# Kernel optimization log

Hardware: AMD Instinct MI355X
Metric: run time of the kernel (lower is better)

Reference implementation:

```python
import jax, jax.numpy as jnp
import numpy as np

N_ROI, N_GRAPHS, HID, EDIM, EMB, NGRP = 116, 128, 64, 5, 16, 4
IN_CH, OUT_CH, N_LAYERS = 116, 2, 2


def _seg_softmax(scores, seg, num_segments):
    # numerically stable softmax over edges grouped by target node
    m = jax.ops.segment_max(scores, seg, num_segments=num_segments)
    ex = jnp.exp(scores - m[seg])
    s = jax.ops.segment_sum(ex, seg, num_segments=num_segments)
    return ex / (s[seg] + 1e-16)


def setup_inputs():
    key = jax.random.key(0)
    ks = jax.random.split(key, 16)
    N = N_ROI * N_GRAPHS
    idx = np.arange(N_ROI)
    s = np.repeat(idx, N_ROI)
    d = np.tile(idx, N_ROI)
    off = (np.arange(N_GRAPHS) * N_ROI)[:, None]
    src = (s[None, :] + off).reshape(-1)
    dst = (d[None, :] + off).reshape(-1)
    E = src.size

    def W(i, shp):
        fan = shp[-2] if len(shp) >= 2 else shp[-1]
        return jax.random.normal(ks[i], shp, jnp.float32) / np.sqrt(fan)

    def z(*shp):
        return jnp.zeros(shp, jnp.float32)

    return {
        "x": jax.random.normal(ks[0], (N, IN_CH), jnp.float32),
        "edge_attr": jax.random.normal(ks[1], (E, EDIM), jnp.float32),
        "emb": W(2, (NGRP, EMB)),
        "enc_W": W(3, (IN_CH + EMB, HID)), "enc_b": z(HID),
        "bn_g": jnp.ones((HID,), jnp.float32), "bn_b": z(HID),
        "gine_We": W(4, (EDIM, HID)), "gine_be": z(HID),
        "gine_W1": W(5, (HID, HID)), "gine_b1": z(HID),
        "gine_W2": W(6, (HID, HID)), "gine_b2": z(HID),
        "gat_Wl": W(7, (N_LAYERS, HID, HID)), "gat_bl": z(N_LAYERS, HID),
        "gat_Wr": W(8, (N_LAYERS, HID, HID)), "gat_br": z(N_LAYERS, HID),
        "gat_att": W(9, (N_LAYERS, HID)),
        "gat_We": W(10, (N_LAYERS, EDIM, HID)),
        "gat_bias": z(N_LAYERS, HID),
        "pool_W1": W(11, (HID, HID)), "pool_b1": z(HID), "pool_w2": W(12, (HID,)),
        "lin1_W": W(13, (HID, IN_CH)), "lin1_b": z(IN_CH),
        "lin2_W": W(14, (IN_CH, OUT_CH)), "lin2_b": z(OUT_CH),
        "edge_index": jnp.asarray(np.stack([src, dst]), jnp.int32),
        "batch": jnp.asarray(np.repeat(np.arange(N_GRAPHS), N_ROI), jnp.int32),
        "group_ids": jnp.asarray(np.tile(idx // 29, N_GRAPHS), jnp.int32),
        "num_graphs": N_GRAPHS,
    }


def reference(x, edge_attr, emb, enc_W, enc_b, bn_g, bn_b,
              gine_We, gine_be, gine_W1, gine_b1, gine_W2, gine_b2,
              gat_Wl, gat_bl, gat_Wr, gat_br, gat_att, gat_We, gat_bias,
              pool_W1, pool_b1, pool_w2, lin1_W, lin1_b, lin2_W, lin2_b,
              edge_index, batch, group_ids, num_graphs):
    src, dst = edge_index[0], edge_index[1]
    N = x.shape[0]
    # BrainEncodeEmbed: concat group embedding, linear, batchnorm (batch stats)
    h = jnp.concatenate([x, emb[group_ids]], axis=-1)          # [N, IN_CH+EMB]
    h = jax.nn.relu(h @ enc_W + enc_b)                          # [N, HID]
    mu = h.mean(0)
    var = h.var(0)
    h = (h - mu) * jax.lax.rsqrt(var + 1e-5) * bn_g + bn_b
    # GINEConv (eps=0): sum_j relu(x_j + lin_edge(e_ij)), then MLP
    e = edge_attr @ gine_We + gine_be                           # [E, HID]
    agg = jax.ops.segment_sum(jax.nn.relu(h[src] + e), dst, num_segments=N)
    h = h + agg
    h = jax.nn.relu(h @ gine_W1 + gine_b1) @ gine_W2 + gine_b2
    h = jax.nn.relu(h)
    # GATv2 layers (heads=1, concat=False)
    for l in range(N_LAYERS):
        xl = h @ gat_Wl[l] + gat_bl[l]                          # [N, HID]
        xr = h @ gat_Wr[l] + gat_br[l]
        zed = jax.nn.leaky_relu(xl[src] + xr[dst] + edge_attr @ gat_We[l], 0.2)
        alpha = _seg_softmax(zed @ gat_att[l], dst, N)          # [E]
        h = jax.nn.relu(
            jax.ops.segment_sum(xl[src] * alpha[:, None], dst, num_segments=N)
            + gat_bias[l])
    # AttentionPooling: global softmax over all nodes, scatter-add by graph
    w = jax.nn.softmax(jnp.tanh(h @ pool_W1 + pool_b1) @ pool_w2, axis=0)
    pooled = jax.ops.segment_sum(h * w[:, None], batch, num_segments=num_graphs)
    return jax.nn.relu(pooled @ lin1_W + lin1_b) @ lin2_W + lin2_b
```

## Files before the change

### kernel.cpp

```cpp
#include <hip/hip_runtime.h>
#include <math.h>

#define R    116
#define R2   (116*116)
#define G    128
#define NN   (R*G)
#define HID  64
#define EDIM 5
#define INCH 116
#define EMBD 16

__device__ __forceinline__ float waveReduceSum(float v) {
#pragma unroll
    for (int m = 32; m >= 1; m >>= 1) v += __shfl_xor(v, m, 64);
    return v;
}

__global__ __launch_bounds__(256) void k_etr(
    const float* __restrict__ ea, float* __restrict__ eat) {
    int b = blockIdx.x;
    int g = b >> 4;
    int t = b & 15;
    int i0 = (t >> 2) << 5, j0 = (t & 3) << 5;
    int ni = min(32, R - i0), nj = min(32, R - j0);
    __shared__ float tile[32][165];
    const float* src = ea + ((size_t)(g*R + i0)*R + j0)*EDIM;
    int tot = ni * nj * EDIM;
    for (int idx = threadIdx.x; idx < tot; idx += 256) {
        int ii = idx / (nj*EDIM);
        int rem = idx - ii*(nj*EDIM);
        tile[ii][rem] = src[(size_t)ii*R*EDIM + rem];
    }
    __syncthreads();
    float* dst = eat + ((size_t)(g*R + j0)*R + i0)*EDIM;
    int tot2 = nj * ni * EDIM;
    for (int idx = threadIdx.x; idx < tot2; idx += 256) {
        int jj = idx / (ni*EDIM);
        int rem = idx - jj*(ni*EDIM);
        int ii = rem / EDIM, e = rem - ii*EDIM;
        dst[(size_t)jj*R*EDIM + rem] = tile[ii][jj*EDIM + e];
    }
}

__global__ __launch_bounds__(64) void k_prep(
    const float* __restrict__ We, const float* __restrict__ att,
    float* __restrict__ wepack, float* __restrict__ was2) {
    int l = blockIdx.x, c = threadIdx.x;
    const float* Wl = We + l*EDIM*HID;
    const float* al = att + l*HID;
    float g0=Wl[c], g1=Wl[64+c], g2=Wl[128+c], g3=Wl[192+c], g4=Wl[256+c];
    float at = al[c];
    float* wp = wepack + l*HID*8 + c*8;
    wp[0]=g0; wp[1]=g1; wp[2]=g2; wp[3]=g3; wp[4]=g4; wp[5]=at;
    wp[6]=0.f; wp[7]=0.f;
    float p0 = waveReduceSum(g0*at);
    float p1 = waveReduceSum(g1*at);
    float p2 = waveReduceSum(g2*at);
    float p3 = waveReduceSum(g3*at);
    float p4 = waveReduceSum(g4*at);
    if (c == 0) {
        float* ws = was2 + l*8;
        ws[0]=p0; ws[1]=p1; ws[2]=p2; ws[3]=p3; ws[4]=p4;
    }
}

__global__ __launch_bounds__(256) void k_encode(
    const float* __restrict__ x, const float* __restrict__ emb,
    const int* __restrict__ group_ids,
    const float* __restrict__ W, const float* __restrict__ bvec,
    float* __restrict__ h) {
    int w = threadIdx.x >> 6, lane = threadIdx.x & 63;
    int n = blockIdx.x*4 + w;
    __shared__ float xin[4][136];
    for (int idx = lane; idx < INCH; idx += 64) xin[w][idx] = x[(size_t)n*INCH + idx];
    if (lane < EMBD) xin[w][INCH + lane] = emb[group_ids[n]*EMBD + lane];
    float acc = bvec[lane];
#pragma unroll
    for (int k = 0; k < INCH + EMBD; k += 4) {
        float4 q = *(const float4*)&xin[w][k];
        acc = fmaf(q.x, W[(k  )*HID + lane], acc);
        acc = fmaf(q.y, W[(k+1)*HID + lane], acc);
        acc = fmaf(q.z, W[(k+2)*HID + lane], acc);
        acc = fmaf(q.w, W[(k+3)*HID + lane], acc);
    }
    h[(size_t)n*HID + lane] = fmaxf(acc, 0.f);
}

__global__ __launch_bounds__(256) void k_stats_partial(
    const float* __restrict__ h, float* __restrict__ partials) {
    int b = blockIdx.x;
    int tid = threadIdx.x;
    int c = tid & 63, r0 = tid >> 6;
    float s = 0.f, s2 = 0.f;
    int row0 = b*64;
#pragma unroll
    for (int k = 0; k < 16; ++k) {
        float v = h[(size_t)(row0 + r0 + 4*k)*HID + c];
        s += v; s2 += v*v;
    }
    __shared__ float ls[256], l2[256];
    ls[tid] = s; l2[tid] = s2;
    __syncthreads();
    if (tid < 64) {
        s  = ls[tid] + ls[tid+64] + ls[tid+128] + ls[tid+192];
        s2 = l2[tid] + l2[tid+64] + l2[tid+128] + l2[tid+192];
        partials[b*128 + tid]      = s;
        partials[b*128 + 64 + tid] = s2;
    }
}

__global__ __launch_bounds__(64) void k_stats_final(
    const float* __restrict__ partials, const float* __restrict__ gam,
    const float* __restrict__ bet, float* __restrict__ stats) {
    int c = threadIdx.x;
    float s = 0.f, s2 = 0.f;
    for (int b = 0; b < NN/64; ++b) {
        s  += partials[b*128 + c];
        s2 += partials[b*128 + 64 + c];
    }
    float mu  = s / (float)NN;
    float var = s2 / (float)NN - mu*mu;
    float rs  = rsqrtf(var + 1e-5f);
    float sc  = rs * gam[c];
    stats[c]      = sc;
    stats[64 + c] = bet[c] - mu*sc;
}

__global__ __launch_bounds__(256) void k_gine(
    const float* __restrict__ h, const float* __restrict__ stats,
    const float* __restrict__ ea,
    const float* __restrict__ We, const float* __restrict__ be,
    const float* __restrict__ W1, const float* __restrict__ b1,
    const float* __restrict__ W2, const float* __restrict__ b2,
    float* __restrict__ hout) {
    int b = blockIdx.x;
    int g = b & (G-1), q = b >> 7;
    int tid = threadIdx.x, w = tid >> 6, lane = tid & 63;
    int j0 = min(q*32 + w*8, R - 8);
    __shared__ float hs[R][64];
    __shared__ float t1s[4][68];
    size_t hbase = (size_t)g*R*HID;
    float scv = stats[lane], shv = stats[64 + lane];
    for (int idx = tid; idx < R*HID; idx += 256)
        hs[idx>>6][lane] = fmaf(h[hbase + idx], scv, shv);
    float w0=We[lane], w1v=We[64+lane], w2v=We[128+lane],
          w3v=We[192+lane], w4v=We[256+lane], bec=be[lane];
    __syncthreads();

    float acc[8] = {0.f,0.f,0.f,0.f,0.f,0.f,0.f,0.f};
    int sbase = __builtin_amdgcn_readfirstlane((g*R*R + j0)*EDIM);
    for (int i = 0; i < R; ++i) {
        float hv = hs[i][lane];
        const float* sp = ea + sbase + i*(R*EDIM);
#pragma unroll
        for (int j = 0; j < 8; ++j) {
            float ew = bec;
            ew = fmaf(sp[j*5+0], w0,  ew);
            ew = fmaf(sp[j*5+1], w1v, ew);
            ew = fmaf(sp[j*5+2], w2v, ew);
            ew = fmaf(sp[j*5+3], w3v, ew);
            ew = fmaf(sp[j*5+4], w4v, ew);
            acc[j] += fmaxf(hv + ew, 0.f);
        }
    }
#pragma unroll
    for (int j = 0; j < 8; ++j) {
        int jd = j0 + j;
        float h1 = hs[jd][lane] + acc[j];
        t1s[w][lane] = h1;
        float a1 = b1[lane];
#pragma unroll
        for (int k = 0; k < HID; k += 4) {
            float4 tq = *(const float4*)&t1s[w][k];
            a1 = fmaf(tq.x, W1[(k  )*HID + lane], a1);
            a1 = fmaf(tq.y, W1[(k+1)*HID + lane], a1);
            a1 = fmaf(tq.z, W1[(k+2)*HID + lane], a1);
            a1 = fmaf(tq.w, W1[(k+3)*HID + lane], a1);
        }
        t1s[w][lane] = fmaxf(a1, 0.f);
        float a2 = b2[lane];
#pragma unroll
        for (int k = 0; k < HID; k += 4) {
            float4 tq = *(const float4*)&t1s[w][k];
            a2 = fmaf(tq.x, W2[(k  )*HID + lane], a2);
            a2 = fmaf(tq.y, W2[(k+1)*HID + lane], a2);
            a2 = fmaf(tq.z, W2[(k+2)*HID + lane], a2);
            a2 = fmaf(tq.w, W2[(k+3)*HID + lane], a2);
        }
        hout[hbase + (size_t)jd*HID + lane] = fmaxf(a2, 0.f);
    }
}

__global__ __launch_bounds__(256) void k_xlxr(
    const float* __restrict__ h,
    const float* __restrict__ Wl, const float* __restrict__ bl,
    const float* __restrict__ Wr, const float* __restrict__ br,
    const float* __restrict__ att,
    float* __restrict__ xl, float* __restrict__ xr,
    float* __restrict__ axl, float* __restrict__ axr) {
    int w = threadIdx.x >> 6, lane = threadIdx.x & 63;
    int n = blockIdx.x*4 + w;
    __shared__ float hr[4][68];
    hr[w][lane] = h[(size_t)n*HID + lane];
    float aL = bl[lane], aR = br[lane];
#pragma unroll
    for (int k = 0; k < HID; k += 4) {
        float4 q = *(const float4*)&hr[w][k];
        aL = fmaf(q.x, Wl[(k  )*HID + lane], aL);
        aR = fmaf(q.x, Wr[(k  )*HID + lane], aR);
        aL = fmaf(q.y, Wl[(k+1)*HID + lane], aL);
        aR = fmaf(q.y, Wr[(k+1)*HID + lane], aR);
        aL = fmaf(q.z, Wl[(k+2)*HID + lane], aL);
        aR = fmaf(q.z, Wr[(k+2)*HID + lane], aR);
        aL = fmaf(q.w, Wl[(k+3)*HID + lane], aL);
        aR = fmaf(q.w, Wr[(k+3)*HID + lane], aR);
    }
    xl[(size_t)n*HID + lane] = aL;
    xr[(size_t)n*HID + lane] = aR;
    float at = att[lane];
    float pL = waveReduceSum(aL * at);
    float pR = waveReduceSum(aR * at);
    if (lane == 0) { axl[n] = pL; axr[n] = pR; }
}

__global__ __launch_bounds__(256) void k_gat(
    const float* __restrict__ xl, const float* __restrict__ xr,
    const float* __restrict__ axlg, const float* __restrict__ axrg,
    const float* __restrict__ eat, const float* __restrict__ wepack,
    const float* __restrict__ wasg, const float* __restrict__ bias,
    float* __restrict__ hout) {
    int b = blockIdx.x;
    int g = b & (G-1), chunk = b >> 7;
    int j0 = chunk*15, jcnt = min(15, R - j0);
    int tid = threadIdx.x, w = tid >> 6, lane = tid & 63;
    __shared__ float xls[R][66];
    __shared__ float ps[4][120];
    size_t hbase = (size_t)g*R*HID;
    for (int idx = tid; idx < R*HID; idx += 256)
        xls[idx>>6][idx&63] = xl[hbase + idx];
    float biasv = bias[lane];
    float wasv0 = wasg[0], wasv1 = wasg[1], wasv2 = wasg[2],
          wasv3 = wasg[3], wasv4 = wasg[4];
    bool vB = lane < (R - 64);
    int rb = vB ? (64 + lane) : lane;
    float axA = axlg[g*R + lane];
    float axB = axlg[g*R + rb];
    __syncthreads();

    for (int jj = w; jj < jcnt; jj += 4) {
        int j = j0 + jj;
        const float* colp = eat + (size_t)(g*R + j)*R*EDIM;
        float eA[5], eB[5];
#pragma unroll
        for (int e = 0; e < 5; ++e) {
            eA[e] = colp[lane*EDIM + e];
            eB[e] = colp[rb*EDIM + e];
        }
        const float* xrp = xr + hbase + (size_t)j*HID;
        float axrj = axrg[g*R + j];
        float accA = 0.f, accB = 0.f;
#pragma unroll 4
        for (int c = 0; c < HID; c += 2) {
            float2 xA2 = *(const float2*)&xls[lane][c];
            float2 xB2 = *(const float2*)&xls[rb][c];
            {
                const float* wp = wepack + c*8;
                float u = xrp[c];
                float zA = xA2.x + u;
                zA = fmaf(eA[0],wp[0],zA); zA = fmaf(eA[1],wp[1],zA);
                zA = fmaf(eA[2],wp[2],zA); zA = fmaf(eA[3],wp[3],zA);
                zA = fmaf(eA[4],wp[4],zA);
                accA = fmaf(__builtin_fabsf(zA), wp[5], accA);
                float zB = xB2.x + u;
                zB = fmaf(eB[0],wp[0],zB); zB = fmaf(eB[1],wp[1],zB);
                zB = fmaf(eB[2],wp[2],zB); zB = fmaf(eB[3],wp[3],zB);
                zB = fmaf(eB[4],wp[4],zB);
                accB = fmaf(__builtin_fabsf(zB), wp[5], accB);
            }
            {
                const float* wp = wepack + (c+1)*8;
                float u = xrp[c+1];
                float zA = xA2.y + u;
                zA = fmaf(eA[0],wp[0],zA); zA = fmaf(eA[1],wp[1],zA);
                zA = fmaf(eA[2],wp[2],zA); zA = fmaf(eA[3],wp[3],zA);
                zA = fmaf(eA[4],wp[4],zA);
                accA = fmaf(__builtin_fabsf(zA), wp[5], accA);
                float zB = xB2.y + u;
                zB = fmaf(eB[0],wp[0],zB); zB = fmaf(eB[1],wp[1],zB);
                zB = fmaf(eB[2],wp[2],zB); zB = fmaf(eB[3],wp[3],zB);
                zB = fmaf(eB[4],wp[4],zB);
                accB = fmaf(__builtin_fabsf(zB), wp[5], accB);
            }
        }
        float LA = axA + axrj, LB = axB + axrj;
        LA = fmaf(eA[0],wasv0,LA); LA = fmaf(eA[1],wasv1,LA);
        LA = fmaf(eA[2],wasv2,LA); LA = fmaf(eA[3],wasv3,LA);
        LA = fmaf(eA[4],wasv4,LA);
        LB = fmaf(eB[0],wasv0,LB); LB = fmaf(eB[1],wasv1,LB);
        LB = fmaf(eB[2],wasv2,LB); LB = fmaf(eB[3],wasv3,LB);
        LB = fmaf(eB[4],wasv4,LB);
        float sA = fmaf(0.4f, accA, 0.6f*LA);
        float sB = vB ? fmaf(0.4f, accB, 0.6f*LB) : -1e30f;
        float m = fmaxf(sA, sB);
#pragma unroll
        for (int msk = 32; msk >= 1; msk >>= 1) m = fmaxf(m, __shfl_xor(m, msk, 64));
        float eAx = __expf(sA - m);
        float eBx = vB ? __expf(sB - m) : 0.f;
        float s = eAx + eBx;
#pragma unroll
        for (int msk = 32; msk >= 1; msk >>= 1) s += __shfl_xor(s, msk, 64);
        float inv = 1.f / (s + 1e-16f);
        ps[w][lane] = eAx * inv;
        if (vB) ps[w][64 + lane] = eBx * inv;
        float o = 0.f;
#pragma unroll 4
        for (int i = 0; i < R; i += 4) {
            float4 p4 = *(const float4*)&ps[w][i];
            o = fmaf(p4.x, xls[i  ][lane], o);
            o = fmaf(p4.y, xls[i+1][lane], o);
            o = fmaf(p4.z, xls[i+2][lane], o);
            o = fmaf(p4.w, xls[i+3][lane], o);
        }
        hout[hbase + (size_t)j*HID + lane] = fmaxf(o + biasv, 0.f);
    }
}

__global__ __launch_bounds__(256) void k_pool_score(
    const float* __restrict__ h, const float* __restrict__ W1,
    const float* __restrict__ b1, const float* __restrict__ w2,
    float* __restrict__ scores) {
    int w = threadIdx.x >> 6, lane = threadIdx.x & 63;
    int n = blockIdx.x*4 + w;
    __shared__ float hr[4][68];
    hr[w][lane] = h[(size_t)n*HID + lane];
    float acc = b1[lane];
#pragma unroll
    for (int k = 0; k < HID; k += 4) {
        float4 q = *(const float4*)&hr[w][k];
        acc = fmaf(q.x, W1[(k  )*HID + lane], acc);
        acc = fmaf(q.y, W1[(k+1)*HID + lane], acc);
        acc = fmaf(q.z, W1[(k+2)*HID + lane], acc);
        acc = fmaf(q.w, W1[(k+3)*HID + lane], acc);
    }
    float p = tanhf(acc) * w2[lane];
    p = waveReduceSum(p);
    if (lane == 0) scores[n] = p;
}

__global__ __launch_bounds__(1024) void k_pool_reduce(
    const float* __restrict__ scores, float* __restrict__ ms) {
    __shared__ float red[1024];
    int tid = threadIdx.x;
    float m = -1e30f;
    for (int i = tid; i < NN; i += 1024) m = fmaxf(m, scores[i]);
    red[tid] = m;
    __syncthreads();
    for (int s = 512; s > 0; s >>= 1) {
        if (tid < s) red[tid] = fmaxf(red[tid], red[tid+s]);
        __syncthreads();
    }
    float mx = red[0];
    __syncthreads();
    float sum = 0.f;
    for (int i = tid; i < NN; i += 1024) sum += __expf(scores[i] - mx);
    red[tid] = sum;
    __syncthreads();
    for (int s = 512; s > 0; s >>= 1) {
        if (tid < s) red[tid] += red[tid+s];
        __syncthreads();
    }
    if (tid == 0) { ms[0] = mx; ms[1] = red[0]; }
}

__global__ __launch_bounds__(64) void k_pool_final(
    const float* __restrict__ h, const float* __restrict__ scores,
    const float* __restrict__ ms,
    const float* __restrict__ lin1W, const float* __restrict__ lin1b,
    const float* __restrict__ lin2W, const float* __restrict__ lin2b,
    float* __restrict__ out) {
    int g = blockIdx.x, c = threadIdx.x;
    float mx = ms[0], inv = 1.f / ms[1];
    float pc = 0.f;
    int nb = g*R;
    for (int r = 0; r < R; ++r) {
        float wv = __expf(scores[nb + r] - mx) * inv;
        pc = fmaf(h[(size_t)(nb + r)*HID + c], wv, pc);
    }
    __shared__ float pl[HID];
    __shared__ float t[INCH];
    pl[c] = pc;
    __syncthreads();
    for (int k = c; k < INCH; k += 64) {
        float acc = lin1b[k];
#pragma unroll 8
        for (int q = 0; q < HID; ++q) acc = fmaf(pl[q], lin1W[q*INCH + k], acc);
        t[k] = fmaxf(acc, 0.f);
    }
    __syncthreads();
    if (c < 2) {
        float o = lin2b[c];
        for (int k = 0; k < INCH; ++k) o = fmaf(t[k], lin2W[k*2 + c], o);
        out[g*2 + c] = o;
    }
}

extern "C" void kernel_launch(void* const* d_in, const int* in_sizes, int n_in,
                              void* d_out, int out_size, void* d_ws, size_t ws_size,
                              hipStream_t stream) {
    (void)in_sizes; (void)n_in; (void)out_size; (void)ws_size;
    const float* x        = (const float*)d_in[0];
    const float* edge_attr= (const float*)d_in[1];
    const float* emb      = (const float*)d_in[2];
    const float* enc_W    = (const float*)d_in[3];
    const float* enc_b    = (const float*)d_in[4];
    const float* bn_g     = (const float*)d_in[5];
    const float* bn_b     = (const float*)d_in[6];
    const float* gine_We  = (const float*)d_in[7];
    const float* gine_be  = (const float*)d_in[8];
    const float* gine_W1  = (const float*)d_in[9];
    const float* gine_b1  = (const float*)d_in[10];
    const float* gine_W2  = (const float*)d_in[11];
    const float* gine_b2  = (const float*)d_in[12];
    const float* gat_Wl   = (const float*)d_in[13];
    const float* gat_bl   = (const float*)d_in[14];
    const float* gat_Wr   = (const float*)d_in[15];
    const float* gat_br   = (const float*)d_in[16];
    const float* gat_att  = (const float*)d_in[17];
    const float* gat_We   = (const float*)d_in[18];
    const float* gat_bias = (const float*)d_in[19];
    const float* pool_W1  = (const float*)d_in[20];
    const float* pool_b1  = (const float*)d_in[21];
    const float* pool_w2  = (const float*)d_in[22];
    const float* lin1_W   = (const float*)d_in[23];
    const float* lin1_b   = (const float*)d_in[24];
    const float* lin2_W   = (const float*)d_in[25];
    const float* lin2_b   = (const float*)d_in[26];
    const int*   group_ids= (const int*)d_in[29];
    float* out = (float*)d_out;

    float* w = (float*)d_ws;
    float* eat      = w;
    float* hA       = eat + (size_t)R2*G*EDIM;
    float* hB       = hA + (size_t)NN*HID;
    float* xlb      = hB + (size_t)NN*HID;
    float* xrb      = xlb + (size_t)NN*HID;
    float* axl      = xrb + (size_t)NN*HID;
    float* axr      = axl + NN;
    float* scores   = axr + NN;
    float* partials = scores + NN;
    float* stats    = partials + (NN/64)*128;
    float* pms      = stats + 128;
    float* wepack   = pms + 2;
    float* was2     = wepack + 2*HID*8;

    k_etr<<<G*16, 256, 0, stream>>>(edge_attr, eat);
    k_prep<<<2, 64, 0, stream>>>(gat_We, gat_att, wepack, was2);
    k_encode<<<NN/4, 256, 0, stream>>>(x, emb, group_ids, enc_W, enc_b, hA);
    k_stats_partial<<<NN/64, 256, 0, stream>>>(hA, partials);
    k_stats_final<<<1, 64, 0, stream>>>(partials, bn_g, bn_b, stats);
    k_gine<<<G*4, 256, 0, stream>>>(hA, stats, edge_attr, gine_We, gine_be,
                                    gine_W1, gine_b1, gine_W2, gine_b2, hB);
    k_xlxr<<<NN/4, 256, 0, stream>>>(hB, gat_Wl, gat_bl, gat_Wr, gat_br,
                                     gat_att, xlb, xrb, axl, axr);
    k_gat<<<G*8, 256, 0, stream>>>(xlb, xrb, axl, axr, eat, wepack,
                                   was2, gat_bias, hA);
    k_xlxr<<<NN/4, 256, 0, stream>>>(hA, gat_Wl + HID*HID, gat_bl + HID,
                                     gat_Wr + HID*HID, gat_br + HID,
                                     gat_att + HID, xlb, xrb, axl, axr);
    k_gat<<<G*8, 256, 0, stream>>>(xlb, xrb, axl, axr, eat, wepack + HID*8,
                                   was2 + 8, gat_bias + HID, hB);
    k_pool_score<<<NN/4, 256, 0, stream>>>(hB, pool_W1, pool_b1, pool_w2, scores);
    k_pool_reduce<<<1, 1024, 0, stream>>>(scores, pms);
    k_pool_final<<<G, 64, 0, stream>>>(hB, scores, pms, lin1_W, lin1_b,
                                       lin2_W, lin2_b, out);
}
```

Before: 267.9 us.

## Restructure GINE and GAT kernels around per-column edge loads and lane broadcasts

k_gine now gives each wave one destination node (G*29 blocks) and reads the transposed edge attributes for that column into registers. It then broadcasts each edge's attributes with readlane, replacing the old 8-column sweep over untransposed global attributes and the overlapping j0 clamping. k_gat now processes two destination columns per wave at once, sharing the xls loads, and keeps the softmax probabilities in registers broadcast via readlane instead of going through the ps shared buffer. The aim is more parallelism for the GINE stage and fewer LDS round trips in GAT, at the cost of higher register pressure and many more blocks that each reload the full hs tile.

```diff
diff --git a/kernel.cpp b/kernel.cpp
--- a/kernel.cpp
+++ b/kernel.cpp
@@ -14,6 +14,10 @@
 #pragma unroll
     for (int m = 32; m >= 1; m >>= 1) v += __shfl_xor(v, m, 64);
     return v;
+}
+
+__device__ __forceinline__ float rlane(float v, int i) {
+    return __int_as_float(__builtin_amdgcn_readlane(__float_as_int(v), i));
 }
 
 __global__ __launch_bounds__(256) void k_etr(
@@ -128,15 +132,15 @@
 
 __global__ __launch_bounds__(256) void k_gine(
     const float* __restrict__ h, const float* __restrict__ stats,
-    const float* __restrict__ ea,
+    const float* __restrict__ eat,
     const float* __restrict__ We, const float* __restrict__ be,
     const float* __restrict__ W1, const float* __restrict__ b1,
     const float* __restrict__ W2, const float* __restrict__ b2,
     float* __restrict__ hout) {
     int b = blockIdx.x;
-    int g = b & (G-1), q = b >> 7;
+    int g = b & (G-1), chunk = b >> 7;
     int tid = threadIdx.x, w = tid >> 6, lane = tid & 63;
-    int j0 = min(q*32 + w*8, R - 8);
+    int j = chunk*4 + w;
     __shared__ float hs[R][64];
     __shared__ float t1s[4][68];
     size_t hbase = (size_t)g*R*HID;
@@ -145,50 +149,55 @@
         hs[idx>>6][lane] = fmaf(h[hbase + idx], scv, shv);
     float w0=We[lane], w1v=We[64+lane], w2v=We[128+lane],
           w3v=We[192+lane], w4v=We[256+lane], bec=be[lane];
-    __syncthreads();
-
-    float acc[8] = {0.f,0.f,0.f,0.f,0.f,0.f,0.f,0.f};
-    int sbase = __builtin_amdgcn_readfirstlane((g*R*R + j0)*EDIM);
-    for (int i = 0; i < R; ++i) {
-        float hv = hs[i][lane];
-        const float* sp = ea + sbase + i*(R*EDIM);
-#pragma unroll
-        for (int j = 0; j < 8; ++j) {
-            float ew = bec;
-            ew = fmaf(sp[j*5+0], w0,  ew);
-            ew = fmaf(sp[j*5+1], w1v, ew);
-            ew = fmaf(sp[j*5+2], w2v, ew);
-            ew = fmaf(sp[j*5+3], w3v, ew);
-            ew = fmaf(sp[j*5+4], w4v, ew);
-            acc[j] += fmaxf(hv + ew, 0.f);
-        }
-    }
-#pragma unroll
-    for (int j = 0; j < 8; ++j) {
-        int jd = j0 + j;
-        float h1 = hs[jd][lane] + acc[j];
-        t1s[w][lane] = h1;
-        float a1 = b1[lane];
-#pragma unroll
-        for (int k = 0; k < HID; k += 4) {
-            float4 tq = *(const float4*)&t1s[w][k];
-            a1 = fmaf(tq.x, W1[(k  )*HID + lane], a1);
-            a1 = fmaf(tq.y, W1[(k+1)*HID + lane], a1);
-            a1 = fmaf(tq.z, W1[(k+2)*HID + lane], a1);
-            a1 = fmaf(tq.w, W1[(k+3)*HID + lane], a1);
-        }
-        t1s[w][lane] = fmaxf(a1, 0.f);
-        float a2 = b2[lane];
-#pragma unroll
-        for (int k = 0; k < HID; k += 4) {
-            float4 tq = *(const float4*)&t1s[w][k];
-            a2 = fmaf(tq.x, W2[(k  )*HID + lane], a2);
-            a2 = fmaf(tq.y, W2[(k+1)*HID + lane], a2);
-            a2 = fmaf(tq.z, W2[(k+2)*HID + lane], a2);
-            a2 = fmaf(tq.w, W2[(k+3)*HID + lane], a2);
-        }
-        hout[hbase + (size_t)jd*HID + lane] = fmaxf(a2, 0.f);
-    }
+    const float* col = eat + (size_t)(g*R + j)*R*EDIM;
+    float4 fa; __builtin_memcpy(&fa, col + lane*EDIM, 16);
+    float fa4 = col[lane*EDIM + 4];
+    int ib = 64 + (lane < (R-64) ? lane : (R-64-1));
+    float4 fb; __builtin_memcpy(&fb, col + ib*EDIM, 16);
+    float fb4 = col[ib*EDIM + 4];
+    __syncthreads();
+
+    float agg = 0.f;
+#pragma unroll 4
+    for (int ii = 0; ii < 64; ++ii) {
+        float s0 = rlane(fa.x, ii), s1 = rlane(fa.y, ii), s2 = rlane(fa.z, ii),
+              s3 = rlane(fa.w, ii), s4 = rlane(fa4, ii);
+        float ew = bec;
+        ew = fmaf(s0, w0,  ew); ew = fmaf(s1, w1v, ew); ew = fmaf(s2, w2v, ew);
+        ew = fmaf(s3, w3v, ew); ew = fmaf(s4, w4v, ew);
+        agg += fmaxf(hs[ii][lane] + ew, 0.f);
+    }
+#pragma unroll 4
+    for (int ii = 0; ii < R-64; ++ii) {
+        float s0 = rlane(fb.x, ii), s1 = rlane(fb.y, ii), s2 = rlane(fb.z, ii),
+              s3 = rlane(fb.w, ii), s4 = rlane(fb4, ii);
+        float ew = bec;
+        ew = fmaf(s0, w0,  ew); ew = fmaf(s1, w1v, ew); ew = fmaf(s2, w2v, ew);
+        ew = fmaf(s3, w3v, ew); ew = fmaf(s4, w4v, ew);
+        agg += fmaxf(hs[64+ii][lane] + ew, 0.f);
+    }
+    float h1 = hs[j][lane] + agg;
+    t1s[w][lane] = h1;
+    float a1 = b1[lane];
+#pragma unroll
+    for (int k = 0; k < HID; k += 4) {
+        float4 tq = *(const float4*)&t1s[w][k];
+        a1 = fmaf(tq.x, W1[(k  )*HID + lane], a1);
+        a1 = fmaf(tq.y, W1[(k+1)*HID + lane], a1);
+        a1 = fmaf(tq.z, W1[(k+2)*HID + lane], a1);
+        a1 = fmaf(tq.w, W1[(k+3)*HID + lane], a1);
+    }
+    t1s[w][lane] = fmaxf(a1, 0.f);
+    float a2 = b2[lane];
+#pragma unroll
+    for (int k = 0; k < HID; k += 4) {
+        float4 tq = *(const float4*)&t1s[w][k];
+        a2 = fmaf(tq.x, W2[(k  )*HID + lane], a2);
+        a2 = fmaf(tq.y, W2[(k+1)*HID + lane], a2);
+        a2 = fmaf(tq.z, W2[(k+2)*HID + lane], a2);
+        a2 = fmaf(tq.w, W2[(k+3)*HID + lane], a2);
+    }
+    hout[hbase + (size_t)j*HID + lane] = fmaxf(a2, 0.f);
 }
 
 __global__ __launch_bounds__(256) void k_xlxr(
@@ -231,10 +240,9 @@
     float* __restrict__ hout) {
     int b = blockIdx.x;
     int g = b & (G-1), chunk = b >> 7;
-    int j0 = chunk*15, jcnt = min(15, R - j0);
+    int j0c = chunk*15, jcnt = min(15, R - j0c);
     int tid = threadIdx.x, w = tid >> 6, lane = tid & 63;
     __shared__ float xls[R][66];
-    __shared__ float ps[4][120];
     size_t hbase = (size_t)g*R*HID;
     for (int idx = tid; idx < R*HID; idx += 256)
         xls[idx>>6][idx&63] = xl[hbase + idx];
@@ -247,81 +255,134 @@
     float axB = axlg[g*R + rb];
     __syncthreads();
 
-    for (int jj = w; jj < jcnt; jj += 4) {
-        int j = j0 + jj;
-        const float* colp = eat + (size_t)(g*R + j)*R*EDIM;
-        float eA[5], eB[5];
+    for (int p = 0; p < 2; ++p) {
+        int jj0 = w + 8*p, jj1 = w + 4 + 8*p;
+        bool act0 = jj0 < jcnt, act1 = jj1 < jcnt;
+        int j0 = j0c + (act0 ? jj0 : 0);
+        int j1 = j0c + (act1 ? jj1 : 0);
+        const float* c0 = eat + (size_t)(g*R + j0)*R*EDIM;
+        const float* c1 = eat + (size_t)(g*R + j1)*R*EDIM;
+        float e0A[5], e0B[5], e1A[5], e1B[5];
 #pragma unroll
         for (int e = 0; e < 5; ++e) {
-            eA[e] = colp[lane*EDIM + e];
-            eB[e] = colp[rb*EDIM + e];
+            e0A[e] = c0[lane*EDIM + e];  e0B[e] = c0[rb*EDIM + e];
+            e1A[e] = c1[lane*EDIM + e];  e1B[e] = c1[rb*EDIM + e];
         }
-        const float* xrp = xr + hbase + (size_t)j*HID;
-        float axrj = axrg[g*R + j];
-        float accA = 0.f, accB = 0.f;
+        int xo0 = __builtin_amdgcn_readfirstlane(j0*HID);
+        int xo1 = __builtin_amdgcn_readfirstlane(j1*HID);
+        const float* xr0 = xr + hbase + xo0;
+        const float* xr1 = xr + hbase + xo1;
+        float axr0 = axrg[g*R + j0];
+        float axr1 = axrg[g*R + j1];
+        float acc0A=0.f, acc0B=0.f, acc1A=0.f, acc1B=0.f;
 #pragma unroll 4
         for (int c = 0; c < HID; c += 2) {
             float2 xA2 = *(const float2*)&xls[lane][c];
             float2 xB2 = *(const float2*)&xls[rb][c];
+            const float* wpa = wepack + c*8;
+            const float* wpb = wepack + (c+1)*8;
+            float u0a = xr0[c], u0b = xr0[c+1];
+            float u1a = xr1[c], u1b = xr1[c+1];
             {
-                const float* wp = wepack + c*8;
-                float u = xrp[c];
-                float zA = xA2.x + u;
-                zA = fmaf(eA[0],wp[0],zA); zA = fmaf(eA[1],wp[1],zA);
-                zA = fmaf(eA[2],wp[2],zA); zA = fmaf(eA[3],wp[3],zA);
-                zA = fmaf(eA[4],wp[4],zA);
-                accA = fmaf(__builtin_fabsf(zA), wp[5], accA);
-                float zB = xB2.x + u;
-                zB = fmaf(eB[0],wp[0],zB); zB = fmaf(eB[1],wp[1],zB);
-                zB = fmaf(eB[2],wp[2],zB); zB = fmaf(eB[3],wp[3],zB);
-                zB = fmaf(eB[4],wp[4],zB);
-                accB = fmaf(__builtin_fabsf(zB), wp[5], accB);
+                float zA = xA2.x + u0a;
+                zA = fmaf(e0A[0],wpa[0],zA); zA = fmaf(e0A[1],wpa[1],zA);
+                zA = fmaf(e0A[2],wpa[2],zA); zA = fmaf(e0A[3],wpa[3],zA);
+                zA = fmaf(e0A[4],wpa[4],zA);
+                acc0A = fmaf(__builtin_fabsf(zA), wpa[5], acc0A);
+                float zB = xB2.x + u0a;
+                zB = fmaf(e0B[0],wpa[0],zB); zB = fmaf(e0B[1],wpa[1],zB);
+                zB = fmaf(e0B[2],wpa[2],zB); zB = fmaf(e0B[3],wpa[3],zB);
+                zB = fmaf(e0B[4],wpa[4],zB);
+                acc0B = fmaf(__builtin_fabsf(zB), wpa[5], acc0B);
+                float yA = xA2.x + u1a;
+                yA = fmaf(e1A[0],wpa[0],yA); yA = fmaf(e1A[1],wpa[1],yA);
+                yA = fmaf(e1A[2],wpa[2],yA); yA = fmaf(e1A[3],wpa[3],yA);
+                yA = fmaf(e1A[4],wpa[4],yA);
+                acc1A = fmaf(__builtin_fabsf(yA), wpa[5], acc1A);
+                float yB = xB2.x + u1a;
+                yB = fmaf(e1B[0],wpa[0],yB); yB = fmaf(e1B[1],wpa[1],yB);
+                yB = fmaf(e1B[2],wpa[2],yB); yB = fmaf(e1B[3],wpa[3],yB);
+                yB = fmaf(e1B[4],wpa[4],yB);
+                acc1B = fmaf(__builtin_fabsf(yB), wpa[5], acc1B);
             }
             {
-                const float* wp = wepack + (c+1)*8;
-                float u = xrp[c+1];
-                float zA = xA2.y + u;
-                zA = fmaf(eA[0],wp[0],zA); zA = fmaf(eA[1],wp[1],zA);
-                zA = fmaf(eA[2],wp[2],zA); zA = fmaf(eA[3],wp[3],zA);
-                zA = fmaf(eA[4],wp[4],zA);
-                accA = fmaf(__builtin_fabsf(zA), wp[5], accA);
-                float zB = xB2.y + u;
-                zB = fmaf(eB[0],wp[0],zB); zB = fmaf(eB[1],wp[1],zB);
-                zB = fmaf(eB[2],wp[2],zB); zB = fmaf(eB[3],wp[3],zB);
-                zB = fmaf(eB[4],wp[4],zB);
-                accB = fmaf(__builtin_fabsf(zB), wp[5], accB);
+                float zA = xA2.y + u0b;
+                zA = fmaf(e0A[0],wpb[0],zA); zA = fmaf(e0A[1],wpb[1],zA);
+                zA = fmaf(e0A[2],wpb[2],zA); zA = fmaf(e0A[3],wpb[3],zA);
+                zA = fmaf(e0A[4],wpb[4],zA);
+                acc0A = fmaf(__builtin_fabsf(zA), wpb[5], acc0A);
+                float zB = xB2.y + u0b;
+                zB = fmaf(e0B[0],wpb[0],zB); zB = fmaf(e0B[1],wpb[1],zB);
+                zB = fmaf(e0B[2],wpb[2],zB); zB = fmaf(e0B[3],wpb[3],zB);
+                zB = fmaf(e0B[4],wpb[4],zB);
+                acc0B = fmaf(__builtin_fabsf(zB), wpb[5], acc0B);
+                float yA = xA2.y + u1b;
+                yA = fmaf(e1A[0],wpb[0],yA); yA = fmaf(e1A[1],wpb[1],yA);
+                yA = fmaf(e1A[2],wpb[2],yA); yA = fmaf(e1A[3],wpb[3],yA);
+                yA = fmaf(e1A[4],wpb[4],yA);
+                acc1A = fmaf(__builtin_fabsf(yA), wpb[5], acc1A);
+                float yB = xB2.y + u1b;
+                yB = fmaf(e1B[0],wpb[0],yB); yB = fmaf(e1B[1],wpb[1],yB);
+                yB = fmaf(e1B[2],wpb[2],yB); yB = fmaf(e1B[3],wpb[3],yB);
+                yB = fmaf(e1B[4],wpb[4],yB);
+                acc1B = fmaf(__builtin_fabsf(yB), wpb[5], acc1B);
             }
         }
-        float LA = axA + axrj, LB = axB + axrj;
-        LA = fmaf(eA[0],wasv0,LA); LA = fmaf(eA[1],wasv1,LA);
-        LA = fmaf(eA[2],wasv2,LA); LA = fmaf(eA[3],wasv3,LA);
-        LA = fmaf(eA[4],wasv4,LA);
-        LB = fmaf(eB[0],wasv0,LB); LB = fmaf(eB[1],wasv1,LB);
-        LB = fmaf(eB[2],wasv2,LB); LB = fmaf(eB[3],wasv3,LB);
-        LB = fmaf(eB[4],wasv4,LB);
-        float sA = fmaf(0.4f, accA, 0.6f*LA);
-        float sB = vB ? fmaf(0.4f, accB, 0.6f*LB) : -1e30f;
-        float m = fmaxf(sA, sB);
-#pragma unroll
-        for (int msk = 32; msk >= 1; msk >>= 1) m = fmaxf(m, __shfl_xor(m, msk, 64));
-        float eAx = __expf(sA - m);
-        float eBx = vB ? __expf(sB - m) : 0.f;
-        float s = eAx + eBx;
-#pragma unroll
-        for (int msk = 32; msk >= 1; msk >>= 1) s += __shfl_xor(s, msk, 64);
-        float inv = 1.f / (s + 1e-16f);
-        ps[w][lane] = eAx * inv;
-        if (vB) ps[w][64 + lane] = eBx * inv;
-        float o = 0.f;
+        float L0A = axA + axr0, L0B = axB + axr0;
+        L0A = fmaf(e0A[0],wasv0,L0A); L0A = fmaf(e0A[1],wasv1,L0A);
+        L0A = fmaf(e0A[2],wasv2,L0A); L0A = fmaf(e0A[3],wasv3,L0A);
+        L0A = fmaf(e0A[4],wasv4,L0A);
+        L0B = fmaf(e0B[0],wasv0,L0B); L0B = fmaf(e0B[1],wasv1,L0B);
+        L0B = fmaf(e0B[2],wasv2,L0B); L0B = fmaf(e0B[3],wasv3,L0B);
+        L0B = fmaf(e0B[4],wasv4,L0B);
+        float L1A = axA + axr1, L1B = axB + axr1;
+        L1A = fmaf(e1A[0],wasv0,L1A); L1A = fmaf(e1A[1],wasv1,L1A);
+        L1A = fmaf(e1A[2],wasv2,L1A); L1A = fmaf(e1A[3],wasv3,L1A);
+        L1A = fmaf(e1A[4],wasv4,L1A);
+        L1B = fmaf(e1B[0],wasv0,L1B); L1B = fmaf(e1B[1],wasv1,L1B);
+        L1B = fmaf(e1B[2],wasv2,L1B); L1B = fmaf(e1B[3],wasv3,L1B);
+        L1B = fmaf(e1B[4],wasv4,L1B);
+        float s0A = fmaf(0.4f, acc0A, 0.6f*L0A);
+        float s0B = vB ? fmaf(0.4f, acc0B, 0.6f*L0B) : -1e30f;
+        float m0 = fmaxf(s0A, s0B);
+#pragma unroll
+        for (int k = 32; k >= 1; k >>= 1) m0 = fmaxf(m0, __shfl_xor(m0, k, 64));
+        float x0A = __expf(s0A - m0);
+        float x0B = vB ? __expf(s0B - m0) : 0.f;
+        float sm0 = x0A + x0B;
+#pragma unroll
+        for (int k = 32; k >= 1; k >>= 1) sm0 += __shfl_xor(sm0, k, 64);
+        float inv0 = 1.f / (sm0 + 1e-16f);
+        float p0A = x0A * inv0, p0B = x0B * inv0;
+
+        float s1A = fmaf(0.4f, acc1A, 0.6f*L1A);
+        float s1B = vB ? fmaf(0.4f, acc1B, 0.6f*L1B) : -1e30f;
+        float m1 = fmaxf(s1A, s1B);
+#pragma unroll
+        for (int k = 32; k >= 1; k >>= 1) m1 = fmaxf(m1, __shfl_xor(m1, k, 64));
+        float x1A = __expf(s1A - m1);
+        float x1B = vB ? __expf(s1B - m1) : 0.f;
+        float sm1 = x1A + x1B;
+#pragma unroll
+        for (int k = 32; k >= 1; k >>= 1) sm1 += __shfl_xor(sm1, k, 64);
+        float inv1 = 1.f / (sm1 + 1e-16f);
+        float p1A = x1A * inv1, p1B = x1B * inv1;
+
+        float o0 = 0.f, o1 = 0.f;
+#pragma unroll 8
+        for (int i = 0; i < 64; ++i) {
+            float xv = xls[i][lane];
+            o0 = fmaf(rlane(p0A, i), xv, o0);
+            o1 = fmaf(rlane(p1A, i), xv, o1);
+        }
 #pragma unroll 4
-        for (int i = 0; i < R; i += 4) {
-            float4 p4 = *(const float4*)&ps[w][i];
-            o = fmaf(p4.x, xls[i  ][lane], o);
-            o = fmaf(p4.y, xls[i+1][lane], o);
-            o = fmaf(p4.z, xls[i+2][lane], o);
-            o = fmaf(p4.w, xls[i+3][lane], o);
+        for (int i = 0; i < R-64; ++i) {
+            float xv = xls[64+i][lane];
+            o0 = fmaf(rlane(p0B, i), xv, o0);
+            o1 = fmaf(rlane(p1B, i), xv, o1);
         }
-        hout[hbase + (size_t)j*HID + lane] = fmaxf(o + biasv, 0.f);
+        if (act0) hout[hbase + (size_t)j0*HID + lane] = fmaxf(o0 + biasv, 0.f);
+        if (act1) hout[hbase + (size_t)j1*HID + lane] = fmaxf(o1 + biasv, 0.f);
     }
 }
 
@@ -458,8 +519,8 @@
     k_encode<<<NN/4, 256, 0, stream>>>(x, emb, group_ids, enc_W, enc_b, hA);
     k_stats_partial<<<NN/64, 256, 0, stream>>>(hA, partials);
     k_stats_final<<<1, 64, 0, stream>>>(partials, bn_g, bn_b, stats);
-    k_gine<<<G*4, 256, 0, stream>>>(hA, stats, edge_attr, gine_We, gine_be,
-                                    gine_W1, gine_b1, gine_W2, gine_b2, hB);
+    k_gine<<<G*29, 256, 0, stream>>>(hA, stats, eat, gine_We, gine_be,
+                                     gine_W1, gine_b1, gine_W2, gine_b2, hB);
     k_xlxr<<<NN/4, 256, 0, stream>>>(hB, gat_Wl, gat_bl, gat_Wr, gat_br,
                                      gat_att, xlb, xrb, axl, axr);
     k_gat<<<G*8, 256, 0, stream>>>(xlb, xrb, axl, axr, eat, wepack,
```

Result: no change. 268.6 us (+0.2%).
